# Performance work log

Hardware: AMD Instinct MI355X
Metric: run time of the kernel (lower is better)

The kernel has to match this reference:

```python
import jax, jax.numpy as jnp
import numpy as np

WINDOW_SIZE = 11
SIGMA = 1.5
C1 = 0.01 ** 2
C2 = 0.03 ** 2


def _gaussian_window(channel, dtype):
    # 1D gaussian, normalized, then outer product -> 2D window, expanded per channel
    xs = np.arange(WINDOW_SIZE) - WINDOW_SIZE // 2
    g = np.exp(-(xs.astype(np.float64) ** 2) / (2.0 * SIGMA ** 2))
    g = (g / g.sum()).astype(np.float32)
    w2d = np.outer(g, g)  # [ws, ws]
    w = np.broadcast_to(w2d[None, None], (channel, 1, WINDOW_SIZE, WINDOW_SIZE))
    return jnp.asarray(w, dtype=dtype)


def _depthwise_conv(img, window, channel):
    pad = WINDOW_SIZE // 2
    return jax.lax.conv_general_dilated(
        img, window,
        window_strides=(1, 1),
        padding=[(pad, pad), (pad, pad)],
        dimension_numbers=('NCHW', 'OIHW', 'NCHW'),
        feature_group_count=channel)


def setup_inputs() -> dict:
    key = jax.random.key(0)
    k1, k2 = jax.random.split(key)
    shape = (16, 3, 512, 512)
    x = jax.random.uniform(k1, shape, dtype=jnp.float32)
    y = jax.random.uniform(k2, shape, dtype=jnp.float32)
    return {"x": x, "y": y}


def reference(x, y):
    channel = x.shape[-3]
    window = _gaussian_window(channel, x.dtype)

    mu1 = _depthwise_conv(x, window, channel)
    mu2 = _depthwise_conv(y, window, channel)
    mu1_sq = mu1 * mu1
    mu2_sq = mu2 * mu2
    mu1_mu2 = mu1 * mu2
    sigma1_sq = _depthwise_conv(x * x, window, channel) - mu1_sq
    sigma2_sq = _depthwise_conv(y * y, window, channel) - mu2_sq
    sigma12 = _depthwise_conv(x * y, window, channel) - mu1_mu2

    ssim_map = ((2.0 * mu1_mu2 + C1) * (2.0 * sigma12 + C2)) / (
        (mu1_sq + mu2_sq + C1) * (sigma1_sq + sigma2_sq + C2))
    # DSSIM = 1 - mean(ssim)
    return 1.0 - jnp.mean(ssim_map)
```

## Files before the change

kernel.cpp:

```cpp
#include <hip/hip_runtime.h>


typedef _Float16 half8 __attribute__((ext_vector_type(8)));
typedef _Float16 half4v __attribute__((ext_vector_type(4)));
typedef float f32x4 __attribute__((ext_vector_type(4)));

#define IMG_W   512
#define IMG_H   512
#define NPLANES 48
#define BR      16
#define RAWROWS 26
#define RAWP    528
#define TP      40
#define GRX     (IMG_H / BR)
#define NBLK    (GRX * NPLANES)

__global__ __launch_bounds__(256, 2)
void dssim_main(const float* __restrict__ xin, const float* __restrict__ yin,
                float* __restrict__ partial) {
    __shared__ _Float16 rawU[RAWROWS][RAWP];
    __shared__ _Float16 rawW[RAWROWS][RAWP];
    __shared__ _Float16 ldsT[4][4][16][TP];
    __shared__ float wpart[4];

    const int t    = threadIdx.x;
    const int lane = t & 63;
    const int wid  = t >> 6;
    const int bn   = lane & 15;
    const int jg   = lane >> 4;
    const int r0   = blockIdx.x * BR;
    const size_t pbase = (size_t)blockIdx.y * (IMG_W * IMG_H);
    const float* __restrict__ xp = xin + pbase;
    const float* __restrict__ yp = yin + pbase;

    float ginv;
    {
        float s = 0.f;
#pragma unroll
        for (int i = 0; i < 11; ++i) {
            float d = (float)(i - 5);
            s += expf(-(d * d) * (1.0f / 4.5f));
        }
        ginv = 1.0f / s;
    }

    half8 whF, wvF;
#pragma unroll
    for (int j = 0; j < 8; ++j) {
        const int k = 8 * jg + j;
        const int dh = k - bn - 3;
        const int dv = k - bn;
        float wh = 0.f, wv = 0.f;
        if (dh >= 0 && dh < 11) {
            const float d = (float)(dh - 5);
            wh = ginv * expf(-(d * d) * (1.0f / 4.5f));
        }
        if (dv >= 0 && dv < 11) {
            const float d = (float)(dv - 5);
            wv = ginv * expf(-(d * d) * (1.0f / 4.5f));
        }
        whF[j] = (_Float16)wh;
        wvF[j] = (_Float16)wv;
    }

    if (t < 104) {
        const int rr   = t >> 2;
        const int hw   = (t >> 1) & 1;
        const int side = t & 1;
        _Float16* base = hw ? &rawW[rr][0] : &rawU[rr][0];
        *(half8*)(base + (side ? (RAWP - 8) : 0)) = (half8)(_Float16)0.0f;
    }

#pragma unroll
    for (int it = 0; it < 13; ++it) {
        const int idx = t + (it << 8);
        const int rr  = idx >> 7;
        const int c4  = idx & 127;
        const int gr  = r0 - 5 + rr;
        float4 xv = make_float4(0.f, 0.f, 0.f, 0.f);
        float4 yv = make_float4(0.f, 0.f, 0.f, 0.f);
        if (gr >= 0 && gr < IMG_H) {
            const size_t o = (size_t)gr * IMG_W + (c4 << 2);
            xv = *(const float4*)(xp + o);
            yv = *(const float4*)(yp + o);
        }
        half4v u, w;
        u[0] = (_Float16)(xv.x + yv.x); w[0] = (_Float16)(xv.x - yv.x);
        u[1] = (_Float16)(xv.y + yv.y); w[1] = (_Float16)(xv.y - yv.y);
        u[2] = (_Float16)(xv.z + yv.z); w[2] = (_Float16)(xv.z - yv.z);
        u[3] = (_Float16)(xv.w + yv.w); w[3] = (_Float16)(xv.w - yv.w);
        *(half4v*)&rawU[rr][8 + (c4 << 2)] = u;
        *(half4v*)&rawW[rr][8 + (c4 << 2)] = w;
    }
    __syncthreads();

    const float C1 = 0.0001f, C2 = 0.0009f;
    const f32x4 zf = {0.f, 0.f, 0.f, 0.f};
    float lsum = 0.f;

    for (int i = 0; i < 8; ++i) {
        const int c0 = (wid + 4 * i) << 4;

#pragma unroll
        for (int rt = 0; rt < 2; ++rt) {
            const int rr = 16 * rt + bn;
            const bool valid = rr < RAWROWS;
            const int rrc = valid ? rr : 0;
            half8 aU = *(const half8*)&rawU[rrc][c0 + 8 * jg];
            half8 aW = *(const half8*)&rawW[rrc][c0 + 8 * jg];
            if (!valid) {
                aU = (half8)(_Float16)0.0f;
                aW = (half8)(_Float16)0.0f;
            }
            half8 aU2, aW2;
#pragma unroll
            for (int d = 0; d < 8; ++d) {
                aU2[d] = aU[d] * aU[d];
                aW2[d] = aW[d] * aW[d];
            }
            const f32x4 cU  = __builtin_amdgcn_mfma_f32_16x16x32_f16(aU,  whF, zf, 0, 0, 0);
            const f32x4 cW  = __builtin_amdgcn_mfma_f32_16x16x32_f16(aW,  whF, zf, 0, 0, 0);
            const f32x4 cU2 = __builtin_amdgcn_mfma_f32_16x16x32_f16(aU2, whF, zf, 0, 0, 0);
            const f32x4 cW2 = __builtin_amdgcn_mfma_f32_16x16x32_f16(aW2, whF, zf, 0, 0, 0);

            half4v hU, hW, hU2, hW2;
#pragma unroll
            for (int ii = 0; ii < 4; ++ii) {
                hU[ii]  = (_Float16)cU[ii];
                hW[ii]  = (_Float16)cW[ii];
                hU2[ii] = (_Float16)cU2[ii];
                hW2[ii] = (_Float16)cW2[ii];
            }
            const int kk = 16 * rt + 4 * jg;
            *(half4v*)&ldsT[wid][0][bn][kk] = hU;
            *(half4v*)&ldsT[wid][1][bn][kk] = hW;
            *(half4v*)&ldsT[wid][2][bn][kk] = hU2;
            *(half4v*)&ldsT[wid][3][bn][kk] = hW2;
        }

        const half8 aTU  = *(const half8*)&ldsT[wid][0][bn][8 * jg];
        const half8 aTW  = *(const half8*)&ldsT[wid][1][bn][8 * jg];
        const half8 aTU2 = *(const half8*)&ldsT[wid][2][bn][8 * jg];
        const half8 aTW2 = *(const half8*)&ldsT[wid][3][bn][8 * jg];
        const f32x4 accU = __builtin_amdgcn_mfma_f32_16x16x32_f16(aTU,  wvF, zf, 0, 0, 0);
        const f32x4 accW = __builtin_amdgcn_mfma_f32_16x16x32_f16(aTW,  wvF, zf, 0, 0, 0);
        const f32x4 accP = __builtin_amdgcn_mfma_f32_16x16x32_f16(aTU2, wvF, zf, 0, 0, 0);
        const f32x4 accQ = __builtin_amdgcn_mfma_f32_16x16x32_f16(aTW2, wvF, zf, 0, 0, 0);

#pragma unroll
        for (int ii = 0; ii < 4; ++ii) {
            const float U = accU[ii], W = accW[ii];
            const float P = accP[ii], Q = accQ[ii];
            const float U2 = U * U, W2 = W * W;
            const float A = 0.5f * (U2 + W2);
            const float B = 0.5f * (U2 - W2);
            const float den2 = fmaf(0.5f, P + Q, -A) + C2;
            const float num2 = fmaf(0.5f, P - Q, -B) + C2;
            lsum += (B + C1) * num2 * __builtin_amdgcn_rcpf((A + C1) * den2);
        }
    }

#pragma unroll
    for (int off = 32; off >= 1; off >>= 1)
        lsum += __shfl_down(lsum, off, 64);
    if (lane == 0) wpart[wid] = lsum;
    __syncthreads();
    if (t == 0) {
        partial[(size_t)blockIdx.y * GRX + blockIdx.x] =
            wpart[0] + wpart[1] + wpart[2] + wpart[3];
    }
}

__global__ __launch_bounds__(256)
void dssim_final(const float* __restrict__ partial, float* __restrict__ out) {
    __shared__ double wsum[4];
    double s = 0.0;
    for (int i = threadIdx.x; i < NBLK; i += 256) s += (double)partial[i];
#pragma unroll
    for (int off = 32; off >= 1; off >>= 1)
        s += __shfl_down(s, off, 64);
    if ((threadIdx.x & 63) == 0) wsum[threadIdx.x >> 6] = s;
    __syncthreads();
    if (threadIdx.x == 0) {
        const double tot = wsum[0] + wsum[1] + wsum[2] + wsum[3];
        out[0] = (float)(1.0 - tot / 12582912.0);
    }
}

extern "C" void kernel_launch(void* const* d_in, const int* in_sizes, int n_in,
                              void* d_out, int out_size, void* d_ws, size_t ws_size,
                              hipStream_t stream) {
    const float* x = (const float*)d_in[0];
    const float* y = (const float*)d_in[1];
    float* out = (float*)d_out;
    float* partial = (float*)d_ws;

    dim3 grid(GRX, NPLANES);
    dim3 block(256);
    dssim_main<<<grid, block, 0, stream>>>(x, y, partial);
    dssim_final<<<1, block, 0, stream>>>(partial, out);
}
```

Measured before the change: 56.97 us.

## Load blur inputs directly from global into MFMA fragments and pipeline across tiles

Drops the shared-memory staging of the full 26-row raw tile and its block-wide barrier. Each lane now loads its 8-float row segments straight from global memory into registers, builds the MFMA A-fragments in place, and prefetches the next column tile's loads while the vertical blur of the current tile runs. The transpose buffer gets two slots and the occupancy hint is raised to 3 blocks per CU. In exchange, neighbouring tiles re-read halo columns from global/L2, since overlapping 8-float windows are fetched more than once, and register pressure rises.

```diff
diff --git a/kernel.cpp b/kernel.cpp
--- a/kernel.cpp
+++ b/kernel.cpp
@@ -4,23 +4,20 @@
 typedef _Float16 half8 __attribute__((ext_vector_type(8)));
 typedef _Float16 half4v __attribute__((ext_vector_type(4)));
 typedef float f32x4 __attribute__((ext_vector_type(4)));
+typedef float f32x8 __attribute__((ext_vector_type(8)));
 
 #define IMG_W   512
 #define IMG_H   512
 #define NPLANES 48
 #define BR      16
-#define RAWROWS 26
-#define RAWP    528
 #define TP      40
 #define GRX     (IMG_H / BR)
 #define NBLK    (GRX * NPLANES)
 
-__global__ __launch_bounds__(256, 2)
+__global__ __launch_bounds__(256, 3)
 void dssim_main(const float* __restrict__ xin, const float* __restrict__ yin,
                 float* __restrict__ partial) {
-    __shared__ _Float16 rawU[RAWROWS][RAWP];
-    __shared__ _Float16 rawW[RAWROWS][RAWP];
-    __shared__ _Float16 ldsT[4][4][16][TP];
+    __shared__ _Float16 ldsT[4][2][4][16][TP];
     __shared__ float wpart[4];
 
     const int t    = threadIdx.x;
@@ -63,101 +60,101 @@
         wvF[j] = (_Float16)wv;
     }
 
-    if (t < 104) {
-        const int rr   = t >> 2;
-        const int hw   = (t >> 1) & 1;
-        const int side = t & 1;
-        _Float16* base = hw ? &rawW[rr][0] : &rawU[rr][0];
-        *(half8*)(base + (side ? (RAWP - 8) : 0)) = (half8)(_Float16)0.0f;
+    const int gr0 = r0 - 5 + bn;
+    const bool rowok0 = (gr0 >= 0) && (gr0 < IMG_H);
+    const int gr1 = r0 + 11 + bn;
+    const bool rowok1 = (bn < 10) && (gr1 < IMG_H);
+    const size_t row0 = (size_t)(rowok0 ? gr0 : 0) * IMG_W;
+    const size_t row1 = (size_t)(rowok1 ? gr1 : 0) * IMG_W;
+
+    const f32x8 z8 = {0.f, 0.f, 0.f, 0.f, 0.f, 0.f, 0.f, 0.f};
+    const f32x4 zf = {0.f, 0.f, 0.f, 0.f};
+    const float C1 = 0.0001f, C2 = 0.0009f;
+    float lsum = 0.f;
+
+    f32x8 xs0, ys0, xs1, ys1;
+
+#define LOADI(ii)                                                           \
+    {                                                                       \
+        const int col = (((wid + 4 * (ii)) << 4) + 8 * jg) - 8;             \
+        const bool colok = (col >= 0) && (col < IMG_W);                     \
+        const size_t co = (size_t)(colok ? col : 0);                        \
+        const bool ok0 = colok && rowok0, ok1 = colok && rowok1;            \
+        xs0 = ok0 ? *(const f32x8*)(xp + row0 + co) : z8;                   \
+        ys0 = ok0 ? *(const f32x8*)(yp + row0 + co) : z8;                   \
+        xs1 = ok1 ? *(const f32x8*)(xp + row1 + co) : z8;                   \
+        ys1 = ok1 ? *(const f32x8*)(yp + row1 + co) : z8;                   \
     }
 
+#define HCOMPI(ii)                                                          \
+    {                                                                       \
+        const int slot = (ii) & 1;                                          \
+        _Pragma("unroll")                                                   \
+        for (int rt = 0; rt < 2; ++rt) {                                    \
+            const f32x8 xv = rt ? xs1 : xs0;                                \
+            const f32x8 yv = rt ? ys1 : ys0;                                \
+            half8 aU, aW, aU2, aW2;                                         \
+            _Pragma("unroll")                                               \
+            for (int d = 0; d < 8; ++d) {                                   \
+                aU[d] = (_Float16)(xv[d] + yv[d]);                          \
+                aW[d] = (_Float16)(xv[d] - yv[d]);                          \
+            }                                                               \
+            _Pragma("unroll")                                               \
+            for (int d = 0; d < 8; ++d) {                                   \
+                aU2[d] = aU[d] * aU[d];                                     \
+                aW2[d] = aW[d] * aW[d];                                     \
+            }                                                               \
+            const f32x4 cU  = __builtin_amdgcn_mfma_f32_16x16x32_f16(aU,  whF, zf, 0, 0, 0); \
+            const f32x4 cW  = __builtin_amdgcn_mfma_f32_16x16x32_f16(aW,  whF, zf, 0, 0, 0); \
+            const f32x4 cU2 = __builtin_amdgcn_mfma_f32_16x16x32_f16(aU2, whF, zf, 0, 0, 0); \
+            const f32x4 cW2 = __builtin_amdgcn_mfma_f32_16x16x32_f16(aW2, whF, zf, 0, 0, 0); \
+            half4v hU, hW, hU2, hW2;                                        \
+            _Pragma("unroll")                                               \
+            for (int q = 0; q < 4; ++q) {                                   \
+                hU[q]  = (_Float16)cU[q];                                   \
+                hW[q]  = (_Float16)cW[q];                                   \
+                hU2[q] = (_Float16)cU2[q];                                  \
+                hW2[q] = (_Float16)cW2[q];                                  \
+            }                                                               \
+            const int kk = 16 * rt + 4 * jg;                                \
+            *(half4v*)&ldsT[wid][slot][0][bn][kk] = hU;                     \
+            *(half4v*)&ldsT[wid][slot][1][bn][kk] = hW;                     \
+            *(half4v*)&ldsT[wid][slot][2][bn][kk] = hU2;                    \
+            *(half4v*)&ldsT[wid][slot][3][bn][kk] = hW2;                    \
+        }                                                                   \
+    }
+
+#define VBLURI(ii)                                                          \
+    {                                                                       \
+        const int slot = (ii) & 1;                                          \
+        const half8 aTU  = *(const half8*)&ldsT[wid][slot][0][bn][8 * jg];  \
+        const half8 aTW  = *(const half8*)&ldsT[wid][slot][1][bn][8 * jg];  \
+        const half8 aTU2 = *(const half8*)&ldsT[wid][slot][2][bn][8 * jg];  \
+        const half8 aTW2 = *(const half8*)&ldsT[wid][slot][3][bn][8 * jg];  \
+        const f32x4 accU = __builtin_amdgcn_mfma_f32_16x16x32_f16(aTU,  wvF, zf, 0, 0, 0); \
+        const f32x4 accW = __builtin_amdgcn_mfma_f32_16x16x32_f16(aTW,  wvF, zf, 0, 0, 0); \
+        const f32x4 accP = __builtin_amdgcn_mfma_f32_16x16x32_f16(aTU2, wvF, zf, 0, 0, 0); \
+        const f32x4 accQ = __builtin_amdgcn_mfma_f32_16x16x32_f16(aTW2, wvF, zf, 0, 0, 0); \
+        _Pragma("unroll")                                                   \
+        for (int q = 0; q < 4; ++q) {                                       \
+            const float U = accU[q], W = accW[q];                           \
+            const float P = accP[q], Q = accQ[q];                           \
+            const float U2 = U * U, W2 = W * W;                             \
+            const float A = 0.5f * (U2 + W2);                               \
+            const float B = 0.5f * (U2 - W2);                               \
+            const float den2 = fmaf(0.5f, P + Q, -A) + C2;                  \
+            const float num2 = fmaf(0.5f, P - Q, -B) + C2;                  \
+            lsum += (B + C1) * num2 * __builtin_amdgcn_rcpf((A + C1) * den2); \
+        }                                                                   \
+    }
+
+    LOADI(0);
+    HCOMPI(0);
 #pragma unroll
-    for (int it = 0; it < 13; ++it) {
-        const int idx = t + (it << 8);
-        const int rr  = idx >> 7;
-        const int c4  = idx & 127;
-        const int gr  = r0 - 5 + rr;
-        float4 xv = make_float4(0.f, 0.f, 0.f, 0.f);
-        float4 yv = make_float4(0.f, 0.f, 0.f, 0.f);
-        if (gr >= 0 && gr < IMG_H) {
-            const size_t o = (size_t)gr * IMG_W + (c4 << 2);
-            xv = *(const float4*)(xp + o);
-            yv = *(const float4*)(yp + o);
-        }
-        half4v u, w;
-        u[0] = (_Float16)(xv.x + yv.x); w[0] = (_Float16)(xv.x - yv.x);
-        u[1] = (_Float16)(xv.y + yv.y); w[1] = (_Float16)(xv.y - yv.y);
-        u[2] = (_Float16)(xv.z + yv.z); w[2] = (_Float16)(xv.z - yv.z);
-        u[3] = (_Float16)(xv.w + yv.w); w[3] = (_Float16)(xv.w - yv.w);
-        *(half4v*)&rawU[rr][8 + (c4 << 2)] = u;
-        *(half4v*)&rawW[rr][8 + (c4 << 2)] = w;
-    }
-    __syncthreads();
-
-    const float C1 = 0.0001f, C2 = 0.0009f;
-    const f32x4 zf = {0.f, 0.f, 0.f, 0.f};
-    float lsum = 0.f;
-
     for (int i = 0; i < 8; ++i) {
-        const int c0 = (wid + 4 * i) << 4;
-
-#pragma unroll
-        for (int rt = 0; rt < 2; ++rt) {
-            const int rr = 16 * rt + bn;
-            const bool valid = rr < RAWROWS;
-            const int rrc = valid ? rr : 0;
-            half8 aU = *(const half8*)&rawU[rrc][c0 + 8 * jg];
-            half8 aW = *(const half8*)&rawW[rrc][c0 + 8 * jg];
-            if (!valid) {
-                aU = (half8)(_Float16)0.0f;
-                aW = (half8)(_Float16)0.0f;
-            }
-            half8 aU2, aW2;
-#pragma unroll
-            for (int d = 0; d < 8; ++d) {
-                aU2[d] = aU[d] * aU[d];
-                aW2[d] = aW[d] * aW[d];
-            }
-            const f32x4 cU  = __builtin_amdgcn_mfma_f32_16x16x32_f16(aU,  whF, zf, 0, 0, 0);
-            const f32x4 cW  = __builtin_amdgcn_mfma_f32_16x16x32_f16(aW,  whF, zf, 0, 0, 0);
-            const f32x4 cU2 = __builtin_amdgcn_mfma_f32_16x16x32_f16(aU2, whF, zf, 0, 0, 0);
-            const f32x4 cW2 = __builtin_amdgcn_mfma_f32_16x16x32_f16(aW2, whF, zf, 0, 0, 0);
-
-            half4v hU, hW, hU2, hW2;
-#pragma unroll
-            for (int ii = 0; ii < 4; ++ii) {
-                hU[ii]  = (_Float16)cU[ii];
-                hW[ii]  = (_Float16)cW[ii];
-                hU2[ii] = (_Float16)cU2[ii];
-                hW2[ii] = (_Float16)cW2[ii];
-            }
-            const int kk = 16 * rt + 4 * jg;
-            *(half4v*)&ldsT[wid][0][bn][kk] = hU;
-            *(half4v*)&ldsT[wid][1][bn][kk] = hW;
-            *(half4v*)&ldsT[wid][2][bn][kk] = hU2;
-            *(half4v*)&ldsT[wid][3][bn][kk] = hW2;
-        }
-
-        const half8 aTU  = *(const half8*)&ldsT[wid][0][bn][8 * jg];
-        const half8 aTW  = *(const half8*)&ldsT[wid][1][bn][8 * jg];
-        const half8 aTU2 = *(const half8*)&ldsT[wid][2][bn][8 * jg];
-        const half8 aTW2 = *(const half8*)&ldsT[wid][3][bn][8 * jg];
-        const f32x4 accU = __builtin_amdgcn_mfma_f32_16x16x32_f16(aTU,  wvF, zf, 0, 0, 0);
-        const f32x4 accW = __builtin_amdgcn_mfma_f32_16x16x32_f16(aTW,  wvF, zf, 0, 0, 0);
-        const f32x4 accP = __builtin_amdgcn_mfma_f32_16x16x32_f16(aTU2, wvF, zf, 0, 0, 0);
-        const f32x4 accQ = __builtin_amdgcn_mfma_f32_16x16x32_f16(aTW2, wvF, zf, 0, 0, 0);
-
-#pragma unroll
-        for (int ii = 0; ii < 4; ++ii) {
-            const float U = accU[ii], W = accW[ii];
-            const float P = accP[ii], Q = accQ[ii];
-            const float U2 = U * U, W2 = W * W;
-            const float A = 0.5f * (U2 + W2);
-            const float B = 0.5f * (U2 - W2);
-            const float den2 = fmaf(0.5f, P + Q, -A) + C2;
-            const float num2 = fmaf(0.5f, P - Q, -B) + C2;
-            lsum += (B + C1) * num2 * __builtin_amdgcn_rcpf((A + C1) * den2);
-        }
+        if (i + 1 < 8) LOADI(i + 1);
+        VBLURI(i);
+        if (i + 1 < 8) HCOMPI(i + 1);
     }
 
 #pragma unroll
```

New measurement: 49.01 us. 14.0% less time.
